# Kernel optimization log

Hardware: AMD Instinct MI355X
Metric: run time of the kernel (lower is better)

Reference implementation:

```python
import jax, jax.numpy as jnp
import numpy as np

B, S, F, H, O, L, HORIZON = 64, 512, 512, 1024, 512, 2, 1


def setup_inputs() -> dict:
    key = jax.random.key(0)
    ks = jax.random.split(key, 11)
    s0 = 1.0 / np.sqrt(F + H)   # torch Linear default init scale (uniform-ish)
    s1 = 1.0 / np.sqrt(H + H)
    sf = 1.0 / np.sqrt(H)
    return {
        "x":   jax.random.normal(ks[0], (B, S, F), jnp.float32),
        "Wf0": jax.random.normal(ks[1], (F + H, H), jnp.float32) * s0,
        "bf0": jax.random.normal(ks[2], (H,), jnp.float32) * s0,
        "Wc0": jax.random.normal(ks[3], (F + H, H), jnp.float32) * s0,
        "bc0": jax.random.normal(ks[4], (H,), jnp.float32) * s0,
        "Wf1": jax.random.normal(ks[5], (H + H, H), jnp.float32) * s1,
        "bf1": jax.random.normal(ks[6], (H,), jnp.float32) * s1,
        "Wc1": jax.random.normal(ks[7], (H + H, H), jnp.float32) * s1,
        "bc1": jax.random.normal(ks[8], (H,), jnp.float32) * s1,
        "Wfc": jax.random.normal(ks[9], (H, O), jnp.float32) * sf,
        "bfc": jax.random.normal(ks[10], (O,), jnp.float32) * sf,
    }


def _janet_forward(x, Wf, bf, Wc, bc, Wfc, bfc):
    # x: [B, S, F] -> scan over time with stacked JANET cells.
    xt = jnp.swapaxes(x, 0, 1)  # [S, B, F]
    h0 = tuple(jnp.zeros((x.shape[0], H), x.dtype) for _ in range(L))
    c0 = tuple(jnp.zeros((x.shape[0], H), x.dtype) for _ in range(L))

    def step(carry, x_t):
        hs, cs = carry
        inp = x_t
        new_h, new_c = [], []
        for l in range(L):
            comb = jnp.concatenate([inp, hs[l]], axis=1)      # [B, in+H]
            f_t = jax.nn.sigmoid(comb @ Wf[l] + bf[l])        # forget gate
            c_tilde = jnp.tanh(comb @ Wc[l] + bc[l])
            c_t = f_t * cs[l] + (1.0 - f_t) * c_tilde
            h_t = jnp.tanh(c_t)
            new_h.append(h_t)
            new_c.append(c_t)
            inp = h_t
        return (tuple(new_h), tuple(new_c)), new_h[-1]

    _, h_seq = jax.lax.scan(step, (h0, c0), xt)               # [S, B, H]
    h_seq = jnp.swapaxes(h_seq, 0, 1)                          # [B, S, H]
    tail = h_seq[:, -HORIZON:, :]                              # dropout is eval-mode identity
    return tail @ Wfc + bfc                                    # [B, HORIZON, O]


def reference(x, Wf0, bf0, Wc0, bc0, Wf1, bf1, Wc1, bc1, Wfc, bfc):
    return _janet_forward(x, (Wf0, Wf1), (bf0, bf1), (Wc0, Wc1), (bc0, bc1), Wfc, bfc)
```

## Files before the change

### kernel.cpp

```cpp
#include <hip/hip_runtime.h>
#include <stdint.h>

typedef _Float16 f16;
typedef _Float16 f16x8 __attribute__((ext_vector_type(8)));
typedef float    f32x4 __attribute__((ext_vector_type(4)));

#define Bm 64
#define Ss 512
#define Ff 512
#define Hh 1024
#define Oo 512
#define NWG 256
#define HBh (Bm*Hh)
#define SLOTB (HBh*2)

#define FL0_U32 0
#define FL1_U32 4096
#define NSLOT 513
#define H0F_BYTE ((size_t)65536)
#define H1F_BYTE (H0F_BYTE + (size_t)NSLOT*SLOTB)
#define WSF_NEED (H1F_BYTE + (size_t)NSLOT*SLOTB)

#define MFMA16 __builtin_amdgcn_mfma_f32_16x16x32_f16

__device__ __forceinline__ float sigm(float x){ return 1.0f/(1.0f+__expf(-x)); }
__device__ __forceinline__ float tanhf_(float x){
  x = fminf(15.0f, fmaxf(-15.0f, x));
  float e = __expf(-2.0f*x);
  return (1.0f - e)/(1.0f + e);
}

__global__ void init_fresh(void* ws){
  const uint4 z = {0,0,0,0};
  int idx = blockIdx.x*blockDim.x + threadIdx.x;
  const int total = 4096 + 8192 + 8192;
  for (int i = idx; i < total; i += gridDim.x*blockDim.x) {
    if (i < 4096)        ((uint4*)ws)[i] = z;
    else if (i < 12288)  ((uint4*)((char*)ws + H0F_BYTE))[i-4096]  = z;
    else                 ((uint4*)((char*)ws + H1F_BYTE))[i-12288] = z;
  }
}

__device__ __forceinline__ void setflag(unsigned* p, unsigned v){
  asm volatile("global_atomic_swap %0, %1, off" :: "v"(p), "v"(v) : "memory");
}

__device__ __forceinline__ void poll1(unsigned* wsu, int fb, unsigned tgt, int tid){
  if (tid < 64) {
    const unsigned* p0 = wsu + fb + 16*tid;
    for (;;) {
      unsigned v0;
      asm volatile("global_load_dword %0, %1, off sc0 sc1\n\t"
                   "s_waitcnt vmcnt(0)"
                   : "=&v"(v0) : "v"(p0) : "memory");
      if (__all(v0 >= tgt)) break;
      __builtin_amdgcn_s_sleep(1);
    }
  }
  asm volatile("s_waitcnt vmcnt(0)" ::: "memory");
  __builtin_amdgcn_sched_barrier(0);
  __syncthreads();
}

__device__ __forceinline__ void poll2(unsigned* wsu, int fb0, unsigned tgt0,
                                      int fb1, unsigned tgt1, int tid){
  if (tid < 64) {
    const unsigned* p0 = wsu + fb0 + 16*tid;
    const unsigned* p1 = wsu + fb1 + 16*tid;
    for (;;) {
      unsigned v0, v1;
      asm volatile("global_load_dword %0, %2, off sc0 sc1\n\t"
                   "global_load_dword %1, %3, off sc0 sc1\n\t"
                   "s_waitcnt vmcnt(0)"
                   : "=&v"(v0), "=&v"(v1) : "v"(p0), "v"(p1) : "memory");
      if (__all((v0 >= tgt0) && (v1 >= tgt1))) break;
      __builtin_amdgcn_s_sleep(1);
    }
  }
  asm volatile("s_waitcnt vmcnt(0)" ::: "memory");
  __builtin_amdgcn_sched_barrier(0);
  __syncthreads();
}

#define ISSUE8T(A, P0, P1, P2, P3) asm volatile( \
  "global_load_dwordx4 %0, %8, off offset:-4096\n\t" \
  "global_load_dwordx4 %1, %8, off\n\t" \
  "global_load_dwordx4 %2, %9, off offset:-4096\n\t" \
  "global_load_dwordx4 %3, %9, off\n\t" \
  "global_load_dwordx4 %4, %10, off offset:-4096\n\t" \
  "global_load_dwordx4 %5, %10, off\n\t" \
  "global_load_dwordx4 %6, %11, off offset:-4096\n\t" \
  "global_load_dwordx4 %7, %11, off" \
  : "=&v"(A[0]), "=&v"(A[1]), "=&v"(A[2]), "=&v"(A[3]), \
    "=&v"(A[4]), "=&v"(A[5]), "=&v"(A[6]), "=&v"(A[7]) \
  : "v"(P0), "v"(P1), "v"(P2), "v"(P3) : "memory")

#define WAITV(N) do{ asm volatile("s_waitcnt vmcnt(" #N ")" ::: "memory"); \
                     __builtin_amdgcn_sched_barrier(0x106); }while(0)

#define CONS8D(Aarr, KSB, KSC) do{ \
  _Pragma("unroll") \
  for (int j = 0; j < 8; ++j){ \
    f16x8 bw = ldsA[(size_t)((KSB)+j)*64]; \
    f16x8 cw = ldsA[(size_t)((KSC)+(KSB)+j)*64]; \
    if (j & 1){ aF1 = MFMA16(Aarr[j], bw, aF1, 0,0,0); aC1 = MFMA16(Aarr[j], cw, aC1, 0,0,0); } \
    else      { aF0 = MFMA16(Aarr[j], bw, aF0, 0,0,0); aC0 = MFMA16(Aarr[j], cw, aC0, 0,0,0); } \
  } \
}while(0)

__device__ __forceinline__ f16x8 cvt8(float4 v0, float4 v1){
  f16x8 a;
  a[0]=v0.x; a[1]=v0.y; a[2]=v0.z; a[3]=v0.w;
  a[4]=v1.x; a[5]=v1.y; a[6]=v1.z; a[7]=v1.w;
  return a;
}

__global__ __launch_bounds__(256,1) void janet_persistent(
    const float* __restrict__ x,
    const float* __restrict__ Wf0, const float* __restrict__ bf0,
    const float* __restrict__ Wc0, const float* __restrict__ bc0,
    const float* __restrict__ Wf1, const float* __restrict__ bf1,
    const float* __restrict__ Wc1, const float* __restrict__ bc1,
    const float* __restrict__ Wfc, const float* __restrict__ bfc,
    float* __restrict__ out, void* __restrict__ ws)
{
  __shared__ __align__(16) unsigned char smem[135168];
  __builtin_amdgcn_fence(__ATOMIC_ACQUIRE, "agent");

  unsigned* wsu = (unsigned*)ws;
  char* h0base = (char*)ws + H0F_BYTE;
  char* h1base = (char*)ws + H1F_BYTE;

  const int wid  = blockIdx.x;
  const int tid  = threadIdx.x;
  const bool isL0 = (wid < 128);
  const int half = (wid >> 6) & 1;
  const int lw   = wid & 63;
  const int col0 = lw * 16;
  const int K    = isL0 ? (Ff + Hh) : (2*Hh);
  const int KS   = K >> 5;

  {
    const float* Wg[2] = { isL0 ? Wf0 : Wf1, isL0 ? Wc0 : Wc1 };
    for (int g = 0; g < 2; ++g) {
      const float* W = Wg[g];
      for (int e = tid; e < 16*K; e += 256) {
        int n = e & 15, k = e >> 4;
        float v = W[(size_t)k*Hh + col0 + n];
        int ks = k >> 5, sub = (k >> 3) & 3, j = k & 7;
        int lane = n + (sub << 4);
        int byte = ((g*KS + ks) << 10) + (lane << 4) + (j << 1);
        *(f16*)(smem + byte) = (f16)v;
      }
    }
  }
  __syncthreads();

  const int lane = tid & 63;
  const int wv   = tid >> 6;
  const int rt   = wv & 1;
  const int kh   = wv >> 1;
  const int n    = lane & 15;
  const int kg   = lane >> 4;
  const int e8   = kg * 8;
  const int lrow = rt*16 + n;
  const int grow = half*32 + lrow;
  const int part = n & 3;
  const int rsel = n >> 2;
  const int srowl = rt*16 + 4*kg + rsel;

  const float* bfp = isL0 ? bf0 : bf1;
  const float* bcp = isL0 ? bc0 : bc1;
  const float bfv = bfp[col0 + n];
  const float bcv = bcp[col0 + n];

  const f16x8* ldsA = (const f16x8*)(smem + (size_t)lane*16);
  const size_t rdoff = (size_t)(kg>>1)*2048 + (size_t)half*1024
                     + (size_t)lrow*32 + (size_t)(kg&1)*16 + 4096;
  float* xchgF = (float*)(smem + 131072 + rt*1024 + lane*16);
  float* xchgC = (float*)(smem + 133120 + rt*1024 + lane*16);

  const int fl0 = FL0_U32 + (half*64)*16;
  const int fl1 = FL1_U32 + (half*64)*16;

  f32x4 cst = {0.f,0.f,0.f,0.f};

  if (isL0) {
    for (int t = 0; t < Ss; ++t) {
      f32x4 aF0={0.f,0.f,0.f,0.f}, aF1={0.f,0.f,0.f,0.f};
      f32x4 aC0={0.f,0.f,0.f,0.f}, aC1={0.f,0.f,0.f,0.f};
      const float* xb = x + ((size_t)grow*Ss + (size_t)t)*Ff + (size_t)kh*256 + e8;
      float4 xv0[8], xv1[8];
      #pragma unroll
      for (int i = 0; i < 8; ++i) {
        xv0[i] = *(const float4*)(xb + 32*i);
        xv1[i] = *(const float4*)(xb + 32*i + 4);
      }
      #pragma unroll
      for (int i = 0; i < 8; ++i) {
        f16x8 a  = cvt8(xv0[i], xv1[i]);
        int ks = kh*8 + i;
        f16x8 bw = ldsA[(size_t)ks*64];
        f16x8 cw = ldsA[(size_t)(48 + ks)*64];
        if (i & 1){ aF1 = MFMA16(a, bw, aF1, 0,0,0); aC1 = MFMA16(a, cw, aC1, 0,0,0); }
        else      { aF0 = MFMA16(a, bw, aF0, 0,0,0); aC0 = MFMA16(a, cw, aC0, 0,0,0); }
      }
      poll1(wsu, fl0, (unsigned)t, tid);
      const char* hb = h0base + (size_t)t*SLOTB + rdoff + (size_t)kh*65536;
      f16x8 A0[8], A1[8];
      __builtin_amdgcn_sched_barrier(0);
      ISSUE8T(A0, hb,       hb+8192,  hb+16384, hb+24576);
      ISSUE8T(A1, hb+32768, hb+40960, hb+49152, hb+57344);
      WAITV(8); CONS8D(A0, 16 + kh*16, 48);
      WAITV(0); CONS8D(A1, 24 + kh*16, 48);
      f32x4 pF = aF0 + aF1, pC = aC0 + aC1;
      if (kh == 1) { *(f32x4*)xchgF = pF; *(f32x4*)xchgC = pC; }
      __syncthreads();
      if (kh == 0) {
        pF += *(const f32x4*)xchgF;
        pC += *(const f32x4*)xchgC;
        unsigned cu[4];
        #pragma unroll
        for (int j = 0; j < 4; ++j) {
          float f  = sigm(pF[j] + bfv);
          float ct = tanhf_(pC[j] + bcv);
          cst[j] = f*cst[j] + (1.0f - f)*ct;
          union { _Float16 h; unsigned short u; } cv; cv.h = (f16)tanhf_(cst[j]);
          cu[j] = cv.u;
        }
        unsigned u01 = cu[0] | (cu[1] << 16);
        unsigned u23 = cu[2] | (cu[3] << 16);
        int sb = (kg << 4) + (part << 2);
        unsigned wsel[4];
        #pragma unroll
        for (int i = 0; i < 4; ++i) {
          unsigned w01 = __shfl(u01, sb + i, 64);
          unsigned w23 = __shfl(u23, sb + i, 64);
          unsigned w = (rsel < 2) ? w01 : w23;
          wsel[i] = (rsel & 1) ? (w >> 16) : (w & 0xffffu);
        }
        unsigned d0 = wsel[0] | (wsel[1] << 16);
        unsigned d1 = wsel[2] | (wsel[3] << 16);
        uint64_t dd = (uint64_t)d0 | ((uint64_t)d1 << 32);
        char* hd = h0base + (size_t)(t+1)*SLOTB + (size_t)lw*2048
                 + (size_t)half*1024 + (size_t)srowl*32 + (size_t)part*8;
        asm volatile("global_atomic_swap_x2 %0, %1, off" :: "v"(hd), "v"(dd) : "memory");
      }
      asm volatile("s_waitcnt vmcnt(0)" ::: "memory");
      __syncthreads();
      if (tid == 0) setflag(wsu + FL0_U32 + (half*64 + lw)*16, (unsigned)(t+1));
    }
  } else {
    for (int s = 0; s < Ss; ++s) {
      poll2(wsu, fl0, (unsigned)(s+1), fl1, (unsigned)s, tid);
      f32x4 aF0={0.f,0.f,0.f,0.f}, aF1={0.f,0.f,0.f,0.f};
      f32x4 aC0={0.f,0.f,0.f,0.f}, aC1={0.f,0.f,0.f,0.f};
      const char* hb = (kh == 0)
        ? h0base + (size_t)(s+1)*SLOTB + rdoff
        : h1base + (size_t)s*SLOTB + rdoff;
      f16x8 A0[8], A1[8], A2[8], A3[8];
      __builtin_amdgcn_sched_barrier(0);
      ISSUE8T(A0, hb,       hb+8192,  hb+16384, hb+24576);
      ISSUE8T(A1, hb+32768, hb+40960, hb+49152, hb+57344);
      ISSUE8T(A2, hb+65536, hb+73728, hb+81920, hb+90112);
      ISSUE8T(A3, hb+98304, hb+106496, hb+114688, hb+122880);
      {
        const int kb = kh*32;
        WAITV(24); CONS8D(A0, kb + 0,  64);
        WAITV(16); CONS8D(A1, kb + 8,  64);
        WAITV(8);  CONS8D(A2, kb + 16, 64);
        WAITV(0);  CONS8D(A3, kb + 24, 64);
      }
      f32x4 pF = aF0 + aF1, pC = aC0 + aC1;
      if (kh == 1) { *(f32x4*)xchgF = pF; *(f32x4*)xchgC = pC; }
      __syncthreads();
      if (kh == 0) {
        pF += *(const f32x4*)xchgF;
        pC += *(const f32x4*)xchgC;
        unsigned cu[4];
        #pragma unroll
        for (int j = 0; j < 4; ++j) {
          float f  = sigm(pF[j] + bfv);
          float ct = tanhf_(pC[j] + bcv);
          cst[j] = f*cst[j] + (1.0f - f)*ct;
          union { _Float16 h; unsigned short u; } cv; cv.h = (f16)tanhf_(cst[j]);
          cu[j] = cv.u;
        }
        unsigned u01 = cu[0] | (cu[1] << 16);
        unsigned u23 = cu[2] | (cu[3] << 16);
        int sb = (kg << 4) + (part << 2);
        unsigned wsel[4];
        #pragma unroll
        for (int i = 0; i < 4; ++i) {
          unsigned w01 = __shfl(u01, sb + i, 64);
          unsigned w23 = __shfl(u23, sb + i, 64);
          unsigned w = (rsel < 2) ? w01 : w23;
          wsel[i] = (rsel & 1) ? (w >> 16) : (w & 0xffffu);
        }
        unsigned d0 = wsel[0] | (wsel[1] << 16);
        unsigned d1 = wsel[2] | (wsel[3] << 16);
        uint64_t dd = (uint64_t)d0 | ((uint64_t)d1 << 32);
        char* hd = h1base + (size_t)(s+1)*SLOTB + (size_t)lw*2048
                 + (size_t)half*1024 + (size_t)srowl*32 + (size_t)part*8;
        asm volatile("global_atomic_swap_x2 %0, %1, off" :: "v"(hd), "v"(dd) : "memory");
      }
      asm volatile("s_waitcnt vmcnt(0)" ::: "memory");
      __syncthreads();
      if (tid == 0) setflag(wsu + FL1_U32 + (half*64 + lw)*16, (unsigned)(s+1));
    }
  }

  poll2(wsu, FL1_U32, (unsigned)Ss, FL1_U32 + 64*16, (unsigned)Ss, tid);
  if (tid < 128) {
    const char* fin = h1base + (size_t)Ss*SLOTB;
    const int o = wid*2 + (tid & 1);
    const int b = tid >> 1;
    const char* rowp = fin + (size_t)(b>>5)*1024 + (size_t)(b&31)*32;
    float acc = bfc[o];
    for (int cg = 0; cg < 64; ++cg) {
      f16x8 lo, hi;
      asm volatile("global_load_dwordx4 %0, %2, off sc0 sc1\n\t"
                   "global_load_dwordx4 %1, %2, off offset:16 sc0 sc1\n\t"
                   "s_waitcnt vmcnt(0)"
                   : "=&v"(lo), "=&v"(hi) : "v"(rowp + (size_t)cg*2048) : "memory");
      #pragma unroll
      for (int i = 0; i < 8; ++i) {
        acc += (float)lo[i] * Wfc[(size_t)(cg*16 + i)*Oo + o];
        acc += (float)hi[i] * Wfc[(size_t)(cg*16 + 8 + i)*Oo + o];
      }
    }
    out[(size_t)b*Oo + o] = acc;
  }
}

extern "C" void kernel_launch(void* const* d_in, const int* in_sizes, int n_in,
                              void* d_out, int out_size, void* d_ws, size_t ws_size,
                              hipStream_t stream) {
  const float* x   = (const float*)d_in[0];
  const float* Wf0 = (const float*)d_in[1];
  const float* bf0 = (const float*)d_in[2];
  const float* Wc0 = (const float*)d_in[3];
  const float* bc0 = (const float*)d_in[4];
  const float* Wf1 = (const float*)d_in[5];
  const float* bf1 = (const float*)d_in[6];
  const float* Wc1 = (const float*)d_in[7];
  const float* bc1 = (const float*)d_in[8];
  const float* Wfc = (const float*)d_in[9];
  const float* bfc = (const float*)d_in[10];

  init_fresh<<<64, 256, 0, stream>>>(d_ws);
  janet_persistent<<<NWG, 256, 0, stream>>>(x, Wf0, bf0, Wc0, bc0,
                                            Wf1, bf1, Wc1, bc1, Wfc, bfc,
                                            (float*)d_out, d_ws);
}
```

Baseline: 2.449 ms.

## Split layer-1 K loop so both halves read h0 then h1, overlapping layer-0 dependency

Layer-1 workgroups now split the K dimension so each kh half reads part of layer-0's h and then part of its own previous h, instead of one half reading h0 and the other h1. The h0 part is consumed first. The poll then waits on the next layer-0 step together with the layer-1 step, so the flag wait overlaps with MFMA work. The wave that finalises the gates switches from kh==0 to kh==1, and a sched_barrier is removed in layer 0. The aim is to shorten the serial critical path between the two stacked recurrences, at the cost of a more intricate synchronisation order that must stay correct.

```diff
diff --git a/kernel.cpp b/kernel.cpp
--- a/kernel.cpp
+++ b/kernel.cpp
@@ -208,7 +208,6 @@
       poll1(wsu, fl0, (unsigned)t, tid);
       const char* hb = h0base + (size_t)t*SLOTB + rdoff + (size_t)kh*65536;
       f16x8 A0[8], A1[8];
-      __builtin_amdgcn_sched_barrier(0);
       ISSUE8T(A0, hb,       hb+8192,  hb+16384, hb+24576);
       ISSUE8T(A1, hb+32768, hb+40960, hb+49152, hb+57344);
       WAITV(8); CONS8D(A0, 16 + kh*16, 48);
@@ -251,30 +250,28 @@
       if (tid == 0) setflag(wsu + FL0_U32 + (half*64 + lw)*16, (unsigned)(t+1));
     }
   } else {
+    poll1(wsu, fl0, 1u, tid);
     for (int s = 0; s < Ss; ++s) {
-      poll2(wsu, fl0, (unsigned)(s+1), fl1, (unsigned)s, tid);
       f32x4 aF0={0.f,0.f,0.f,0.f}, aF1={0.f,0.f,0.f,0.f};
       f32x4 aC0={0.f,0.f,0.f,0.f}, aC1={0.f,0.f,0.f,0.f};
-      const char* hb = (kh == 0)
-        ? h0base + (size_t)(s+1)*SLOTB + rdoff
-        : h1base + (size_t)s*SLOTB + rdoff;
-      f16x8 A0[8], A1[8], A2[8], A3[8];
-      __builtin_amdgcn_sched_barrier(0);
-      ISSUE8T(A0, hb,       hb+8192,  hb+16384, hb+24576);
-      ISSUE8T(A1, hb+32768, hb+40960, hb+49152, hb+57344);
-      ISSUE8T(A2, hb+65536, hb+73728, hb+81920, hb+90112);
-      ISSUE8T(A3, hb+98304, hb+106496, hb+114688, hb+122880);
-      {
-        const int kb = kh*32;
-        WAITV(24); CONS8D(A0, kb + 0,  64);
-        WAITV(16); CONS8D(A1, kb + 8,  64);
-        WAITV(8);  CONS8D(A2, kb + 16, 64);
-        WAITV(0);  CONS8D(A3, kb + 24, 64);
-      }
+      const char* hbA = h0base + (size_t)(s+1)*SLOTB + rdoff + (size_t)kh*65536;
+      f16x8 A0[8], A1[8];
+      ISSUE8T(A0, hbA,       hbA+8192,  hbA+16384, hbA+24576);
+      ISSUE8T(A1, hbA+32768, hbA+40960, hbA+49152, hbA+57344);
+      WAITV(8); CONS8D(A0, kh*16,     64);
+      WAITV(0); CONS8D(A1, kh*16 + 8, 64);
+      unsigned f0tgt = (unsigned)(s+2 > Ss ? Ss : s+2);
+      poll2(wsu, fl0, f0tgt, fl1, (unsigned)s, tid);
+      const char* hbB = h1base + (size_t)s*SLOTB + rdoff + (size_t)kh*65536;
+      f16x8 B0[8], B1[8];
+      ISSUE8T(B0, hbB,       hbB+8192,  hbB+16384, hbB+24576);
+      ISSUE8T(B1, hbB+32768, hbB+40960, hbB+49152, hbB+57344);
+      WAITV(8); CONS8D(B0, 32 + kh*16,     64);
+      WAITV(0); CONS8D(B1, 32 + kh*16 + 8, 64);
       f32x4 pF = aF0 + aF1, pC = aC0 + aC1;
-      if (kh == 1) { *(f32x4*)xchgF = pF; *(f32x4*)xchgC = pC; }
+      if (kh == 0) { *(f32x4*)xchgF = pF; *(f32x4*)xchgC = pC; }
       __syncthreads();
-      if (kh == 0) {
+      if (kh == 1) {
         pF += *(const f32x4*)xchgF;
         pC += *(const f32x4*)xchgC;
         unsigned cu[4];
```

New measurement: 2.376 ms. 3.0% less time.
